# Kernel tuning notes

Hardware: AMD Instinct MI355X
Metric: run time of the kernel (lower is better)

The kernel has to match this reference:

```python
import jax, jax.numpy as jnp
import numpy as np

HEADS = 4
C = 128            # per-head out channels (hard-coded 128 in the module)
NEG_SLOPE_ATT = 0.2   # GATConv attention leaky_relu slope
NEG_SLOPE = 0.01      # F.leaky_relu default slope


def _diag_output_ids(num_groups, n):
    # ids = base_i + n*j + j for group i, agent j; base_i = i * n^2
    i = np.arange(num_groups)[:, None] * (n * n)
    j = np.arange(n)[None, :] * (n + 1)
    return jnp.asarray((i + j).reshape(-1))


def setup_inputs() -> dict:
    key = jax.random.key(0)
    ks = jax.random.split(key, 12)
    num_groups, n_agents = 12, 48
    N = num_groups * n_agents * n_agents      # 27648 nodes
    E = 442368
    F_in, edge_dim, hidden = 256, 16, 256
    s = 0.05
    return {
        "x": jax.random.normal(ks[0], (N, F_in), jnp.float32),
        "edge_index": jax.random.randint(ks[1], (2, E), 0, N, jnp.int32),
        "edge_attr": jax.random.normal(ks[2], (E, edge_dim), jnp.float32),
        "num_groups": num_groups,
        "agents_per_group": n_agents,
        "W": jax.random.normal(ks[3], (F_in, HEADS * C), jnp.float32) * s,
        "att_src": jax.random.normal(ks[4], (HEADS, C), jnp.float32) * s,
        "att_dst": jax.random.normal(ks[5], (HEADS, C), jnp.float32) * s,
        "W_edge": jax.random.normal(ks[6], (edge_dim, HEADS * C), jnp.float32) * s,
        "att_edge": jax.random.normal(ks[7], (HEADS, C), jnp.float32) * s,
        "bias_gat": jnp.zeros((HEADS * C,), jnp.float32),
        "fc_W": jax.random.normal(ks[8], (HEADS * C, hidden), jnp.float32) * s,
        "fc_b": jnp.zeros((hidden,), jnp.float32),
    }


def _gat_conv(x, src, dst, edge_attr_full, W, att_src, att_dst, W_edge, att_edge, bias):
    N = x.shape[0]
    h = (x @ W).reshape(N, HEADS, C)                       # [N,H,C]
    a_src = jnp.einsum('nhc,hc->nh', h, att_src)           # [N,H]
    a_dst = jnp.einsum('nhc,hc->nh', h, att_dst)
    he = (edge_attr_full @ W_edge).reshape(-1, HEADS, C)   # [E',H,C]
    a_edge = jnp.einsum('ehc,hc->eh', he, att_edge)
    logits = jax.nn.leaky_relu(a_src[src] + a_dst[dst] + a_edge, NEG_SLOPE_ATT)
    # segment softmax over incoming edges of each dst node
    m = jax.ops.segment_max(logits, dst, num_segments=N)   # [N,H]
    e = jnp.exp(logits - m[dst])
    s = jax.ops.segment_sum(e, dst, num_segments=N)
    alpha = e / (s[dst] + 1e-16)                           # [E',H]
    msg = h[src] * alpha[..., None]                        # [E',H,C]
    out = jax.ops.segment_sum(msg, dst, num_segments=N)    # [N,H,C]
    return out.reshape(N, HEADS * C) + bias


def reference(x, edge_index, edge_attr, num_groups, agents_per_group,
              W, att_src, att_dst, W_edge, att_edge, bias_gat, fc_W, fc_b):
    N = x.shape[0]
    # add self-loops (PyG default), self-loop edge_attr = mean fill
    loops = jnp.arange(N, dtype=edge_index.dtype)
    src = jnp.concatenate([edge_index[0], loops])
    dst = jnp.concatenate([edge_index[1], loops])
    ea = jnp.concatenate([edge_attr,
                          jnp.broadcast_to(edge_attr.mean(0), (N, edge_attr.shape[1]))])
    h = jax.nn.leaky_relu(
        _gat_conv(x, src, dst, ea, W, att_src, att_dst, W_edge, att_edge, bias_gat),
        NEG_SLOPE)
    ids = _diag_output_ids(num_groups, agents_per_group)
    # fc_output + leaky_relu then diagonal index-select (select first: same math)
    return jax.nn.leaky_relu(h[ids] @ fc_W + fc_b, NEG_SLOPE)
```

## Files before the change

### kernel.cpp

```cpp
#include <hip/hip_runtime.h>

#define NNODES 27648
#define NEDGES 442368
#define FIN    256
#define HC     512
#define NH     4
#define CDIM   128
#define NAG    48
#define NGRP   12
#define N2     2304
#define NOUT   576
#define CAP    128
#define EDIM   16
#define MPART  512

__device__ __forceinline__ float lrelu(float v, float s){ return v > 0.0f ? v : s * v; }

__device__ __forceinline__ float wsum(float v){
  #pragma unroll
  for (int off = 32; off; off >>= 1) v += __shfl_xor(v, off, 64);
  return v;
}
__device__ __forceinline__ float wmax(float v){
  #pragma unroll
  for (int off = 32; off; off >>= 1) v = fmaxf(v, __shfl_xor(v, off, 64));
  return v;
}

__global__ __launch_bounds__(256) void k_pre(
    const float* __restrict__ W, const float* __restrict__ att_src,
    const float* __restrict__ att_dst, const float* __restrict__ W_edge,
    const float* __restrict__ att_edge, const float* __restrict__ ea,
    float* __restrict__ ws_, float* __restrict__ wd_, float* __restrict__ we_,
    int* __restrict__ counts, float4* __restrict__ easum_part){
  int b = blockIdx.x;
  int tid = threadIdx.x;
  if (b < 11) {
    int g = b * 256 + tid;
    if (g < 1024) {
      int f = g >> 2, h = g & 3;
      const float4* wp = (const float4*)(W + f*HC + h*CDIM);
      const float4* ap = (const float4*)(att_src + h*CDIM);
      float s = 0.f;
      #pragma unroll 8
      for (int c4 = 0; c4 < CDIM/4; c4++){
        float4 wv = wp[c4], av = ap[c4];
        s += wv.x*av.x + wv.y*av.y + wv.z*av.z + wv.w*av.w;
      }
      ws_[g] = s;
    } else if (g < 2048) {
      int gg = g - 1024; int f = gg >> 2, h = gg & 3;
      const float4* wp = (const float4*)(W + f*HC + h*CDIM);
      const float4* ap = (const float4*)(att_dst + h*CDIM);
      float s = 0.f;
      #pragma unroll 8
      for (int c4 = 0; c4 < CDIM/4; c4++){
        float4 wv = wp[c4], av = ap[c4];
        s += wv.x*av.x + wv.y*av.y + wv.z*av.z + wv.w*av.w;
      }
      wd_[gg] = s;
    } else if (g < 2112) {
      int gg = g - 2048; int d = gg >> 2, h = gg & 3;
      const float4* wp = (const float4*)(W_edge + d*HC + h*CDIM);
      const float4* ap = (const float4*)(att_edge + h*CDIM);
      float s = 0.f;
      #pragma unroll 8
      for (int c4 = 0; c4 < CDIM/4; c4++){
        float4 wv = wp[c4], av = ap[c4];
        s += wv.x*av.x + wv.y*av.y + wv.z*av.z + wv.w*av.w;
      }
      we_[gg] = s;
    } else if (g < 2112 + NOUT) {
      counts[g - 2112] = 0;
    }
  } else {
    int pb = b - 11;
    const float4* p = (const float4*)ea;
    const int total = NEDGES * 4;
    float4 acc = make_float4(0.f, 0.f, 0.f, 0.f);
    for (int i = pb*256 + tid; i < total; i += MPART*256){
      float4 v = p[i];
      acc.x += v.x; acc.y += v.y; acc.z += v.z; acc.w += v.w;
    }
    #pragma unroll
    for (int off = 4; off <= 32; off <<= 1){
      acc.x += __shfl_xor(acc.x, off, 64);
      acc.y += __shfl_xor(acc.y, off, 64);
      acc.z += __shfl_xor(acc.z, off, 64);
      acc.w += __shfl_xor(acc.w, off, 64);
    }
    __shared__ float4 sd4[16];
    int lane = tid & 63, wave = tid >> 6;
    if (lane < 4) sd4[wave*4 + lane] = acc;
    __syncthreads();
    if (tid < 4){
      float4 t = sd4[tid];
      float4 a = sd4[4+tid], c = sd4[8+tid], d = sd4[12+tid];
      t.x += a.x + c.x + d.x; t.y += a.y + c.y + d.y;
      t.z += a.z + c.z + d.z; t.w += a.w + c.w + d.w;
      easum_part[pb*4 + tid] = t;
    }
  }
}

__global__ __launch_bounds__(256) void k_scan(const int* __restrict__ ei,
    const float* __restrict__ ea, const float* __restrict__ we_,
    int* __restrict__ counts, int* __restrict__ slist, float* __restrict__ aed,
    const float* __restrict__ easum_part, float* __restrict__ easum){
  int tid = threadIdx.x;
  if (blockIdx.x == NEDGES/256){
    int col = tid & 15, part = tid >> 4;
    float s = 0.f;
    for (int pb = 0; pb < MPART/16; pb++)
      s += easum_part[(part*(MPART/16) + pb)*16 + col];
    __shared__ float sd[256];
    sd[tid] = s;
    __syncthreads();
    if (tid < 16){
      float t = 0.f;
      #pragma unroll
      for (int i = 0; i < 16; i++) t += sd[i*16 + tid];
      easum[tid] = t;
    }
    return;
  }
  int e = blockIdx.x*256 + tid;
  int dst = ei[NEDGES + e];
  int r = dst % N2;
  if (r % 49) return;
  int row = (dst / N2) * NAG + r / 49;
  int pos = atomicAdd(&counts[row], 1);
  if (pos >= CAP) return;
  slist[row*CAP + pos] = ei[e];
  const float* eap = ea + (size_t)e*EDIM;
  float a0=0.f,a1=0.f,a2=0.f,a3=0.f;
  #pragma unroll
  for (int d = 0; d < EDIM; d++){
    float v = eap[d];
    a0 += v*we_[d*4+0]; a1 += v*we_[d*4+1]; a2 += v*we_[d*4+2]; a3 += v*we_[d*4+3];
  }
  float* ap = aed + (size_t)(row*CAP+pos)*4;
  ap[0]=a0; ap[1]=a1; ap[2]=a2; ap[3]=a3;
}

__global__ __launch_bounds__(256) void k_attn(const float* __restrict__ x,
    const float* __restrict__ ws_, const float* __restrict__ wd_,
    const float* __restrict__ we_, const float* __restrict__ easum,
    const int* __restrict__ counts, const int* __restrict__ slist,
    const float* __restrict__ aed, float* __restrict__ z){
  __shared__ float lg[(CAP+1)*4];
  __shared__ int   srcs[CAP];
  __shared__ float adst_s[4];
  int row = blockIdx.x;
  int g = row / NAG, j = row - g*NAG;
  int dst = g*N2 + j*49;
  int tid = threadIdx.x;
  int lane = tid & 63, wave = tid >> 6;
  int k = counts[row]; if (k > CAP) k = CAP;

  float wsr[4][4];
  #pragma unroll
  for (int q = 0; q < 4; q++){
    float4 t = *(const float4*)(ws_ + (lane*4+q)*4);
    wsr[q][0]=t.x; wsr[q][1]=t.y; wsr[q][2]=t.z; wsr[q][3]=t.w;
  }

  for (int i = wave; i < k; i += 4){
    int src = slist[row*CAP + i];
    float4 aedv = *(const float4*)(aed + (size_t)(row*CAP+i)*4);
    float4 xv = *(const float4*)(x + (size_t)src*FIN + lane*4);
    float p0 = xv.x*wsr[0][0] + xv.y*wsr[1][0] + xv.z*wsr[2][0] + xv.w*wsr[3][0];
    float p1 = xv.x*wsr[0][1] + xv.y*wsr[1][1] + xv.z*wsr[2][1] + xv.w*wsr[3][1];
    float p2 = xv.x*wsr[0][2] + xv.y*wsr[1][2] + xv.z*wsr[2][2] + xv.w*wsr[3][2];
    float p3 = xv.x*wsr[0][3] + xv.y*wsr[1][3] + xv.z*wsr[2][3] + xv.w*wsr[3][3];
    p0 = wsum(p0); p1 = wsum(p1); p2 = wsum(p2); p3 = wsum(p3);
    if (lane == 0){
      srcs[i] = src;
      lg[i*4+0] = p0 + aedv.x; lg[i*4+1] = p1 + aedv.y;
      lg[i*4+2] = p2 + aedv.z; lg[i*4+3] = p3 + aedv.w;
    }
  }

  if (wave == 0){
    float wdr[4][4];
    #pragma unroll
    for (int q = 0; q < 4; q++){
      float4 t = *(const float4*)(wd_ + (lane*4+q)*4);
      wdr[q][0]=t.x; wdr[q][1]=t.y; wdr[q][2]=t.z; wdr[q][3]=t.w;
    }
    float4 xv = *(const float4*)(x + (size_t)dst*FIN + lane*4);
    float pd[4], ps[4];
    #pragma unroll
    for (int h = 0; h < 4; h++){
      pd[h] = xv.x*wdr[0][h] + xv.y*wdr[1][h] + xv.z*wdr[2][h] + xv.w*wdr[3][h];
      ps[h] = xv.x*wsr[0][h] + xv.y*wsr[1][h] + xv.z*wsr[2][h] + xv.w*wsr[3][h];
    }
    const float invE = 1.0f/(float)NEDGES;
    float md = (lane < 16) ? easum[lane]*invE : 0.f;
    float al[4];
    #pragma unroll
    for (int h = 0; h < 4; h++){
      float c = (lane < 16) ? md*we_[lane*4+h] : 0.f;
      al[h] = wsum(c);
      pd[h] = wsum(pd[h]);
      ps[h] = wsum(ps[h]);
    }
    if (lane == 0){
      #pragma unroll
      for (int h = 0; h < 4; h++){
        adst_s[h] = pd[h];
        lg[k*4+h] = ps[h] + al[h];
      }
    }
  }
  __syncthreads();

  {
    int h = wave;
    float ad = adst_s[h];
    float m = -1e30f;
    for (int i = lane; i <= k; i += 64){
      float v = lrelu(lg[i*4+h] + ad, 0.2f);
      lg[i*4+h] = v;
      m = fmaxf(m, v);
    }
    m = wmax(m);
    float s = 0.f;
    for (int i = lane; i <= k; i += 64){
      float e = __expf(lg[i*4+h] - m);
      lg[i*4+h] = e;
      s += e;
    }
    s = wsum(s);
    float inv = 1.0f/(s + 1e-16f);
    for (int i = lane; i <= k; i += 64) lg[i*4+h] *= inv;
  }
  __syncthreads();

  int f = tid;
  float a0=0.f,a1=0.f,a2=0.f,a3=0.f;
  for (int i = 0; i < k; i++){
    float xv = x[(size_t)srcs[i]*FIN + f];
    a0 += lg[i*4+0]*xv; a1 += lg[i*4+1]*xv; a2 += lg[i*4+2]*xv; a3 += lg[i*4+3]*xv;
  }
  {
    float xv = x[(size_t)dst*FIN + f];
    a0 += lg[k*4+0]*xv; a1 += lg[k*4+1]*xv; a2 += lg[k*4+2]*xv; a3 += lg[k*4+3]*xv;
  }
  float* zp = z + (size_t)row*1024;
  zp[0*256+f]=a0; zp[1*256+f]=a1; zp[2*256+f]=a2; zp[3*256+f]=a3;
}

__global__ __launch_bounds__(256) void k_gemm1(const float* __restrict__ z,
    const float* __restrict__ W, const float* __restrict__ bias,
    float* __restrict__ h2){
  __shared__ float zs[8*256];
  int base = blockIdx.x * 8;
  int h = blockIdx.y;
  int tid = threadIdx.x;
  for (int idx = tid; idx < 2048; idx += 256){
    int r = idx >> 8, f = idx & 255;
    zs[idx] = z[(size_t)(base+r)*1024 + h*256 + f];
  }
  __syncthreads();
  int c = tid & 127, rq = tid >> 7;
  float acc0=0.f, acc1=0.f, acc2=0.f, acc3=0.f;
  const float* Wp = W + h*CDIM + c;
  for (int f0 = 0; f0 < 256; f0 += 4){
    float w0 = Wp[(size_t)(f0+0)*HC];
    float w1 = Wp[(size_t)(f0+1)*HC];
    float w2 = Wp[(size_t)(f0+2)*HC];
    float w3 = Wp[(size_t)(f0+3)*HC];
    float4 z0 = *(const float4*)&zs[(rq*4+0)*256 + f0];
    float4 z1 = *(const float4*)&zs[(rq*4+1)*256 + f0];
    float4 z2 = *(const float4*)&zs[(rq*4+2)*256 + f0];
    float4 z3 = *(const float4*)&zs[(rq*4+3)*256 + f0];
    acc0 += z0.x*w0 + z0.y*w1 + z0.z*w2 + z0.w*w3;
    acc1 += z1.x*w0 + z1.y*w1 + z1.z*w2 + z1.w*w3;
    acc2 += z2.x*w0 + z2.y*w1 + z2.z*w2 + z2.w*w3;
    acc3 += z3.x*w0 + z3.y*w1 + z3.z*w2 + z3.w*w3;
  }
  int o = h*CDIM + c;
  float b = bias[o];
  h2[(size_t)(base + rq*4 + 0)*HC + o] = lrelu(acc0 + b, 0.01f);
  h2[(size_t)(base + rq*4 + 1)*HC + o] = lrelu(acc1 + b, 0.01f);
  h2[(size_t)(base + rq*4 + 2)*HC + o] = lrelu(acc2 + b, 0.01f);
  h2[(size_t)(base + rq*4 + 3)*HC + o] = lrelu(acc3 + b, 0.01f);
}

__global__ __launch_bounds__(256) void k_gemm2(const float* __restrict__ h2,
    const float* __restrict__ fcW, const float* __restrict__ fcb,
    float* __restrict__ out){
  __shared__ float hs[4*512];
  int base = blockIdx.x * 4;
  int tid = threadIdx.x;
  for (int idx = tid; idx < 2048; idx += 256){
    hs[idx] = h2[(size_t)base*HC + idx];
  }
  __syncthreads();
  int j = tid;
  float acc0=0.f, acc1=0.f, acc2=0.f, acc3=0.f;
  for (int k0 = 0; k0 < 512; k0 += 4){
    float w0 = fcW[(size_t)(k0+0)*256 + j];
    float w1 = fcW[(size_t)(k0+1)*256 + j];
    float w2 = fcW[(size_t)(k0+2)*256 + j];
    float w3 = fcW[(size_t)(k0+3)*256 + j];
    float4 h0 = *(const float4*)&hs[0*512 + k0];
    float4 h1 = *(const float4*)&hs[1*512 + k0];
    float4 h2v = *(const float4*)&hs[2*512 + k0];
    float4 h3 = *(const float4*)&hs[3*512 + k0];
    acc0 += h0.x*w0 + h0.y*w1 + h0.z*w2 + h0.w*w3;
    acc1 += h1.x*w0 + h1.y*w1 + h1.z*w2 + h1.w*w3;
    acc2 += h2v.x*w0 + h2v.y*w1 + h2v.z*w2 + h2v.w*w3;
    acc3 += h3.x*w0 + h3.y*w1 + h3.z*w2 + h3.w*w3;
  }
  float b = fcb[j];
  out[(size_t)(base+0)*256 + j] = lrelu(acc0 + b, 0.01f);
  out[(size_t)(base+1)*256 + j] = lrelu(acc1 + b, 0.01f);
  out[(size_t)(base+2)*256 + j] = lrelu(acc2 + b, 0.01f);
  out[(size_t)(base+3)*256 + j] = lrelu(acc3 + b, 0.01f);
}

extern "C" void kernel_launch(void* const* d_in, const int* in_sizes, int n_in,
                              void* d_out, int out_size, void* d_ws, size_t ws_size,
                              hipStream_t stream) {
  const float* x        = (const float*)d_in[0];
  const int*   ei       = (const int*)  d_in[1];
  const float* ea       = (const float*)d_in[2];
  const float* W        = (const float*)d_in[5];
  const float* att_src  = (const float*)d_in[6];
  const float* att_dst  = (const float*)d_in[7];
  const float* W_edge   = (const float*)d_in[8];
  const float* att_edge = (const float*)d_in[9];
  const float* bias     = (const float*)d_in[10];
  const float* fcW      = (const float*)d_in[11];
  const float* fcb      = (const float*)d_in[12];
  float* out = (float*)d_out;

  float* w = (float*)d_ws;
  float*  ws_       = w;
  float*  wd_       = w + 1024;
  float*  we_       = w + 2048;
  float*  easum     = w + 2112;
  int*    counts    = (int*)(w + 2128);
  float*  easum_p   = w + 2704;
  int*    slist     = (int*)(w + 10896);
  float*  aed       = w + 84624;
  float*  z         = w + 379536;
  float*  h2        = w + 969360;

  k_pre<<<11 + MPART, 256, 0, stream>>>(W, att_src, att_dst, W_edge, att_edge, ea,
                                        ws_, wd_, we_, counts, (float4*)easum_p);
  k_scan<<<NEDGES/256 + 1, 256, 0, stream>>>(ei, ea, we_, counts, slist, aed,
                                             easum_p, easum);
  k_attn<<<NOUT, 256, 0, stream>>>(x, ws_, wd_, we_, easum, counts, slist, aed, z);
  k_gemm1<<<dim3(72,4), 256, 0, stream>>>(z, W, bias, h2);
  k_gemm2<<<144, 256, 0, stream>>>(h2, fcW, fcb, out);
}
```

Before: 163.8 us.

## Fuse attention aggregation and both GEMMs into one per-row kernel

Merges k_attn, k_gemm1 and k_gemm2 into a single kernel where each block keeps its aggregated z row and hidden row in shared memory and runs both matrix-vector products locally. This removes two kernel launches and the global round-trips of z and h2. In exchange, each block now reads the full W (512 KB) and fcW (512 KB) for one row, with no reuse across rows, so weight traffic rises from L2 and per-block work lengthens.

```diff
diff --git a/kernel.cpp b/kernel.cpp
--- a/kernel.cpp
+++ b/kernel.cpp
@@ -143,14 +143,19 @@
   ap[0]=a0; ap[1]=a1; ap[2]=a2; ap[3]=a3;
 }
 
-__global__ __launch_bounds__(256) void k_attn(const float* __restrict__ x,
+__global__ __launch_bounds__(256) void k_mega(const float* __restrict__ x,
     const float* __restrict__ ws_, const float* __restrict__ wd_,
     const float* __restrict__ we_, const float* __restrict__ easum,
     const int* __restrict__ counts, const int* __restrict__ slist,
-    const float* __restrict__ aed, float* __restrict__ z){
+    const float* __restrict__ aed,
+    const float* __restrict__ W, const float* __restrict__ bias,
+    const float* __restrict__ fcW, const float* __restrict__ fcb,
+    float* __restrict__ out){
   __shared__ float lg[(CAP+1)*4];
   __shared__ int   srcs[CAP];
   __shared__ float adst_s[4];
+  __shared__ float zs[4*256];
+  __shared__ float hs[512];
   int row = blockIdx.x;
   int g = row / NAG, j = row - g*NAG;
   int dst = g*N2 + j*49;
@@ -237,88 +242,51 @@
   }
   __syncthreads();
 
-  int f = tid;
-  float a0=0.f,a1=0.f,a2=0.f,a3=0.f;
-  for (int i = 0; i < k; i++){
-    float xv = x[(size_t)srcs[i]*FIN + f];
-    a0 += lg[i*4+0]*xv; a1 += lg[i*4+1]*xv; a2 += lg[i*4+2]*xv; a3 += lg[i*4+3]*xv;
-  }
   {
-    float xv = x[(size_t)dst*FIN + f];
-    a0 += lg[k*4+0]*xv; a1 += lg[k*4+1]*xv; a2 += lg[k*4+2]*xv; a3 += lg[k*4+3]*xv;
-  }
-  float* zp = z + (size_t)row*1024;
-  zp[0*256+f]=a0; zp[1*256+f]=a1; zp[2*256+f]=a2; zp[3*256+f]=a3;
-}
-
-__global__ __launch_bounds__(256) void k_gemm1(const float* __restrict__ z,
-    const float* __restrict__ W, const float* __restrict__ bias,
-    float* __restrict__ h2){
-  __shared__ float zs[8*256];
-  int base = blockIdx.x * 8;
-  int h = blockIdx.y;
-  int tid = threadIdx.x;
-  for (int idx = tid; idx < 2048; idx += 256){
-    int r = idx >> 8, f = idx & 255;
-    zs[idx] = z[(size_t)(base+r)*1024 + h*256 + f];
+    int f = tid;
+    float a0=0.f,a1=0.f,a2=0.f,a3=0.f;
+    for (int i = 0; i < k; i++){
+      float xv = x[(size_t)srcs[i]*FIN + f];
+      a0 += lg[i*4+0]*xv; a1 += lg[i*4+1]*xv; a2 += lg[i*4+2]*xv; a3 += lg[i*4+3]*xv;
+    }
+    {
+      float xv = x[(size_t)dst*FIN + f];
+      a0 += lg[k*4+0]*xv; a1 += lg[k*4+1]*xv; a2 += lg[k*4+2]*xv; a3 += lg[k*4+3]*xv;
+    }
+    zs[0*256+f]=a0; zs[1*256+f]=a1; zs[2*256+f]=a2; zs[3*256+f]=a3;
   }
   __syncthreads();
-  int c = tid & 127, rq = tid >> 7;
-  float acc0=0.f, acc1=0.f, acc2=0.f, acc3=0.f;
-  const float* Wp = W + h*CDIM + c;
-  for (int f0 = 0; f0 < 256; f0 += 4){
-    float w0 = Wp[(size_t)(f0+0)*HC];
-    float w1 = Wp[(size_t)(f0+1)*HC];
-    float w2 = Wp[(size_t)(f0+2)*HC];
-    float w3 = Wp[(size_t)(f0+3)*HC];
-    float4 z0 = *(const float4*)&zs[(rq*4+0)*256 + f0];
-    float4 z1 = *(const float4*)&zs[(rq*4+1)*256 + f0];
-    float4 z2 = *(const float4*)&zs[(rq*4+2)*256 + f0];
-    float4 z3 = *(const float4*)&zs[(rq*4+3)*256 + f0];
-    acc0 += z0.x*w0 + z0.y*w1 + z0.z*w2 + z0.w*w3;
-    acc1 += z1.x*w0 + z1.y*w1 + z1.z*w2 + z1.w*w3;
-    acc2 += z2.x*w0 + z2.y*w1 + z2.z*w2 + z2.w*w3;
-    acc3 += z3.x*w0 + z3.y*w1 + z3.z*w2 + z3.w*w3;
-  }
-  int o = h*CDIM + c;
-  float b = bias[o];
-  h2[(size_t)(base + rq*4 + 0)*HC + o] = lrelu(acc0 + b, 0.01f);
-  h2[(size_t)(base + rq*4 + 1)*HC + o] = lrelu(acc1 + b, 0.01f);
-  h2[(size_t)(base + rq*4 + 2)*HC + o] = lrelu(acc2 + b, 0.01f);
-  h2[(size_t)(base + rq*4 + 3)*HC + o] = lrelu(acc3 + b, 0.01f);
-}
-
-__global__ __launch_bounds__(256) void k_gemm2(const float* __restrict__ h2,
-    const float* __restrict__ fcW, const float* __restrict__ fcb,
-    float* __restrict__ out){
-  __shared__ float hs[4*512];
-  int base = blockIdx.x * 4;
-  int tid = threadIdx.x;
-  for (int idx = tid; idx < 2048; idx += 256){
-    hs[idx] = h2[(size_t)base*HC + idx];
+
+  {
+    int o1 = tid, o2 = tid + 256;
+    const float* z1 = zs + ((tid >> 7) << 8);
+    const float* z2 = zs + 512 + ((tid >> 7) << 8);
+    const float* W1 = W + o1;
+    float acc1 = 0.f, acc2 = 0.f;
+    for (int ff = 0; ff < 256; ff += 8){
+      #pragma unroll
+      for (int u = 0; u < 8; u++){
+        float w1 = W1[(size_t)(ff+u)*HC];
+        float w2 = W1[(size_t)(ff+u)*HC + 256];
+        acc1 += z1[ff+u]*w1;
+        acc2 += z2[ff+u]*w2;
+      }
+    }
+    hs[o1] = lrelu(acc1 + bias[o1], 0.01f);
+    hs[o2] = lrelu(acc2 + bias[o2], 0.01f);
   }
   __syncthreads();
-  int j = tid;
-  float acc0=0.f, acc1=0.f, acc2=0.f, acc3=0.f;
-  for (int k0 = 0; k0 < 512; k0 += 4){
-    float w0 = fcW[(size_t)(k0+0)*256 + j];
-    float w1 = fcW[(size_t)(k0+1)*256 + j];
-    float w2 = fcW[(size_t)(k0+2)*256 + j];
-    float w3 = fcW[(size_t)(k0+3)*256 + j];
-    float4 h0 = *(const float4*)&hs[0*512 + k0];
-    float4 h1 = *(const float4*)&hs[1*512 + k0];
-    float4 h2v = *(const float4*)&hs[2*512 + k0];
-    float4 h3 = *(const float4*)&hs[3*512 + k0];
-    acc0 += h0.x*w0 + h0.y*w1 + h0.z*w2 + h0.w*w3;
-    acc1 += h1.x*w0 + h1.y*w1 + h1.z*w2 + h1.w*w3;
-    acc2 += h2v.x*w0 + h2v.y*w1 + h2v.z*w2 + h2v.w*w3;
-    acc3 += h3.x*w0 + h3.y*w1 + h3.z*w2 + h3.w*w3;
-  }
-  float b = fcb[j];
-  out[(size_t)(base+0)*256 + j] = lrelu(acc0 + b, 0.01f);
-  out[(size_t)(base+1)*256 + j] = lrelu(acc1 + b, 0.01f);
-  out[(size_t)(base+2)*256 + j] = lrelu(acc2 + b, 0.01f);
-  out[(size_t)(base+3)*256 + j] = lrelu(acc3 + b, 0.01f);
+
+  {
+    const float* Fw = fcW + tid;
+    float acc = 0.f;
+    for (int k0 = 0; k0 < 512; k0 += 8){
+      #pragma unroll
+      for (int u = 0; u < 8; u++)
+        acc += hs[k0+u] * Fw[(size_t)(k0+u)*256];
+    }
+    out[(size_t)row*256 + tid] = lrelu(acc + fcb[tid], 0.01f);
+  }
 }
 
 extern "C" void kernel_launch(void* const* d_in, const int* in_sizes, int n_in,
@@ -346,14 +314,11 @@
   float*  easum_p   = w + 2704;
   int*    slist     = (int*)(w + 10896);
   float*  aed       = w + 84624;
-  float*  z         = w + 379536;
-  float*  h2        = w + 969360;
 
   k_pre<<<11 + MPART, 256, 0, stream>>>(W, att_src, att_dst, W_edge, att_edge, ea,
                                         ws_, wd_, we_, counts, (float4*)easum_p);
   k_scan<<<NEDGES/256 + 1, 256, 0, stream>>>(ei, ea, we_, counts, slist, aed,
                                              easum_p, easum);
-  k_attn<<<NOUT, 256, 0, stream>>>(x, ws_, wd_, we_, easum, counts, slist, aed, z);
-  k_gemm1<<<dim3(72,4), 256, 0, stream>>>(z, W, bias, h2);
-  k_gemm2<<<144, 256, 0, stream>>>(h2, fcW, fcb, out);
-}
+  k_mega<<<NOUT, 256, 0, stream>>>(x, ws_, wd_, we_, easum, counts, slist, aed,
+                                   W, bias, fcW, fcb, out);
+}
```

Result: no change. 161.0 us (-1.7%).
